# Kernel optimization log

Hardware: AMD Instinct MI355X
Metric: run time of the kernel (lower is better)

Reference implementation:

```python
import jax, jax.numpy as jnp
import numpy as np

THRES1 = 0.8      # self.thres1
THRES_UP = 0.5    # self.thres_up
R = 1.0           # self.r
MAX_FRAME = 60    # self.max_frame
SEQ, FEAT = 65536, 512


def _get_thres2(max_frame=MAX_FRAME, thres=0.6):
    # Faithful port of TGNN.get_threshold: grid-search alpha in (0,1] step 0.01
    a = 0.0
    e = 0.01
    min_score = 1e7
    alpha = e
    for _ in range(100):
        a = a + e
        y = 0.0
        for _ in range(max_frame):
            y = a * 1.0 + (1.0 - a) * y
        score = abs(y - thres)
        if min_score > score:
            min_score = score
            alpha = a
    # with up=1, a_ stays == alpha, so y[i] = alpha + (1-alpha)*y[i-1]
    y = 0.0
    ys = []
    for _ in range(max_frame):
        y = alpha + (1.0 - alpha) * y
        ys.append(y)
    return np.asarray(ys, dtype=np.float32)


def setup_inputs() -> dict:
    key = jax.random.key(0)
    k0, k1, k2, k3, k4 = jax.random.split(key, 5)
    h = jax.random.normal(k0, (SEQ, FEAT), jnp.float32)            # per-frame CTR features
    W = jax.random.normal(k1, (FEAT, 1), jnp.float32) / np.float32(np.sqrt(FEAT))
    b = jnp.zeros((1,), jnp.float32)
    u = jax.random.uniform(k2, (SEQ,), jnp.float32)                # batch['u'] (unused in loss, as in torch)
    u_pred = jax.random.uniform(k3, (SEQ,), jnp.float32)           # batch['u_pred']
    label = jax.random.uniform(k4, (SEQ,), jnp.float32)            # batch['y']
    thres2 = jnp.asarray(_get_thres2())
    return {"h": h, "W": W, "b": b, "u": u, "u_pred": u_pred, "label": label, "thres2": thres2}


def reference(h, W, b, u, u_pred, label, thres2):
    # stand-in for self.ctr.calc_alpha(h).squeeze(): per-frame alpha in (0,1)
    a = jax.nn.sigmoid(h @ W + b)[:, 0]                             # [seq]
    seq = a.shape[0]
    idxs = jnp.arange(seq, dtype=jnp.int32)

    def step(carry, xs):
        up_pre, up_max, a_pre, y_pre, l_c, loss, cnt = carry
        i, a_i, up_i, lab_i = xs
        # start_frame is reset to 0 at the top of every torch iteration, so
        # i - start_frame == 0 whenever start_frame > 0 -> that elif never fires,
        # and in the l_e branch start_frame == 0 -> index is simply i.
        cross = (up_pre < THRES_UP) & (up_i >= THRES_UP)
        up_max = jnp.where(cross, up_i, jnp.maximum(up_max, up_i))
        up_hat = jnp.where(up_i >= THRES_UP, up_max, up_i)
        alpha_ = up_hat * a_pre + (1.0 - up_hat) * a_i
        y_ = alpha_ * up_hat + (1.0 - alpha_) * y_pre
        y_ = jnp.where(up_hat < THRES_UP, jnp.float32(0.0), y_)
        # label >= thres1: set pending loss l_c (sentinel -1 if gate closed)
        l_c = jnp.where(lab_i >= THRES1,
                        jnp.where(up_hat < THRES_UP, jnp.float32(-1.0), (y_ - lab_i) ** 2),
                        l_c)
        # falling edge of the gate: flush accumulated loss
        fall = (up_pre >= THRES_UP) & (up_hat < THRES_UP)
        is_neg = l_c == -1.0
        nonzero = l_c != 0.0
        t2 = thres2[jnp.minimum(i, MAX_FRAME - 1)]
        l_e = (y_pre - t2) ** 2
        add_c = fall & (~is_neg) & nonzero
        add_e = fall & (~is_neg) & (~nonzero) & (y_pre >= THRES1)
        loss = loss + jnp.where(add_c, l_c * R, 0.0) + jnp.where(add_e, l_e, 0.0)
        cnt = cnt + (add_c | add_e).astype(jnp.int32)
        l_c = jnp.where(fall, jnp.float32(0.0), l_c)
        return (up_hat, up_max, alpha_, y_, l_c, loss, cnt), (alpha_, up_hat, y_)

    z = jnp.float32(0.0)
    init = (z, z, z, z, z, z, jnp.int32(0))
    (_, _, _, _, _, loss, cnt), (alphas, up_hats, ys) = jax.lax.scan(
        step, init, (idxs, a, u_pred, label))
    return ys, alphas, u_pred, up_hats, loss, cnt
```

## Files before the change

### kernel.cpp

```cpp
#include <hip/hip_runtime.h>
#include <math.h>

#define SEQ 65536
#define FEAT 512
#define NCH 256
#define CHUNK 256
#define THRES1 0.8f
#define THRES_UP 0.5f
#define NEGINF -1e30f

__global__ __launch_bounds__(256) void k_matvec(const float* __restrict__ h,
                                                const float* __restrict__ W,
                                                const float* __restrict__ b,
                                                float* __restrict__ a) {
    int wave = threadIdx.x >> 6;
    int lane = threadIdx.x & 63;
    int row  = blockIdx.x * 4 + wave;
    const float4* hp = (const float4*)(h + (size_t)row * FEAT);
    const float4* wp = (const float4*)W;
    int base = lane * 2;
    float4 h0 = hp[base], h1 = hp[base + 1];
    float4 w0 = wp[base], w1 = wp[base + 1];
    float s = h0.x * w0.x + h0.y * w0.y + h0.z * w0.z + h0.w * w0.w
            + h1.x * w1.x + h1.y * w1.y + h1.z * w1.z + h1.w * w1.w;
    #pragma unroll
    for (int off = 32; off; off >>= 1) s += __shfl_down(s, off, 64);
    if (lane == 0) a[row] = 1.0f / (1.0f + expf(-(s + b[0])));
}

__global__ __launch_bounds__(256) void k_local(const float* __restrict__ u_pred,
                                               const float* __restrict__ label,
                                               float* __restrict__ m_loc, int* __restrict__ openA,
                                               int* __restrict__ ltLoc, int* __restrict__ lfExcl,
                                               float* __restrict__ lastm, int* __restrict__ lastopen,
                                               int* __restrict__ lastgate, int* __restrict__ trigLast,
                                               int* __restrict__ fallLast) {
    __shared__ float su[256];
    __shared__ float sm[256];
    __shared__ int   sr[256];
    __shared__ int   st[256];
    __shared__ int   sf[256];
    int t = threadIdx.x, c = blockIdx.x;
    int i = c * CHUNK + t;
    float u = u_pred[i];
    su[t] = u;
    __syncthreads();
    bool gate = u >= THRES_UP;
    bool gprevLocal = (t > 0) && (su[t - 1] >= THRES_UP);
    bool gprev = (t > 0) ? gprevLocal : ((i > 0) && (u_pred[i - 1] >= THRES_UP));
    bool fall = gprev && !gate;
    bool trig = label[i] >= THRES1;

    sm[t] = gate ? u : NEGINF;
    sr[t] = gate ? ((t > 0 && !gprevLocal) ? 1 : 0) : 1;
    st[t] = trig ? i : -1;
    sf[t] = fall ? i : -1;
    __syncthreads();
    for (int d = 1; d < 256; d <<= 1) {
        float lm = NEGINF; int lr = 0, lt = -1, lf = -1;
        bool act = t >= d;
        if (act) { lm = sm[t - d]; lr = sr[t - d]; lt = st[t - d]; lf = sf[t - d]; }
        __syncthreads();
        if (act) {
            if (!sr[t]) sm[t] = fmaxf(lm, sm[t]);
            sr[t] |= lr;
            st[t] = max(st[t], lt);
            sf[t] = max(sf[t], lf);
        }
        __syncthreads();
    }
    m_loc[i]  = sm[t];
    openA[i]  = (sr[t] == 0 && gate) ? 1 : 0;
    ltLoc[i]  = st[t];
    lfExcl[i] = (t == 0) ? -1 : sf[t - 1];
    if (t == 255) {
        lastm[c]    = sm[255];
        lastopen[c] = (sr[255] == 0 && gate) ? 1 : 0;
        lastgate[c] = gate ? 1 : 0;
        trigLast[c] = st[255];
        fallLast[c] = sf[255];
    }
}

__global__ __launch_bounds__(256) void k_mid1(const float* __restrict__ lastm,
                                              const int* __restrict__ lastopen,
                                              const int* __restrict__ lastgate,
                                              const int* __restrict__ trigLast,
                                              const int* __restrict__ fallLast,
                                              float* __restrict__ inc, int* __restrict__ trigIn,
                                              int* __restrict__ fallIn,
                                              float* __restrict__ losscnt) {
    __shared__ float sA[256], sB[256];
    __shared__ int   st[256], sf[256];
    int t = threadIdx.x;
    bool lg = lastgate[t] != 0;
    sA[t] = lg ? lastm[t] : NEGINF;
    sB[t] = (lg && lastopen[t]) ? 0.0f : NEGINF;
    st[t] = trigLast[t];
    sf[t] = fallLast[t];
    __syncthreads();
    for (int d = 1; d < 256; d <<= 1) {
        float lA = NEGINF, lB = NEGINF; int lt = -1, lf = -1;
        bool act = t >= d;
        if (act) { lA = sA[t - d]; lB = sB[t - d]; lt = st[t - d]; lf = sf[t - d]; }
        __syncthreads();
        if (act) {
            float nA = fmaxf(sA[t], sB[t] + lA);
            float nB = fmaxf(sB[t] + lB, NEGINF);
            sA[t] = nA; sB[t] = nB;
            st[t] = max(st[t], lt);
            sf[t] = max(sf[t], lf);
        }
        __syncthreads();
    }
    inc[t]    = (t == 0) ? NEGINF : fmaxf(sA[t - 1], sB[t - 1] + NEGINF);
    trigIn[t] = (t == 0) ? -1 : st[t - 1];
    fallIn[t] = (t == 0) ? -1 : sf[t - 1];
    if (t == 0) { losscnt[0] = 0.0f; losscnt[1] = 0.0f; }
}

__global__ __launch_bounds__(256) void k_uphat_alpha(const float* __restrict__ u_pred,
                                                     const float* __restrict__ a,
                                                     const float* __restrict__ m_loc,
                                                     const int* __restrict__ openA,
                                                     const float* __restrict__ inc,
                                                     float* __restrict__ Pc, float* __restrict__ Qc,
                                                     float* __restrict__ Pch, float* __restrict__ Qch,
                                                     float* __restrict__ out) {
    __shared__ float sc[256], sd[256];
    int t = threadIdx.x, c = blockIdx.x;
    int i = c * CHUNK + t;
    float u = u_pred[i];
    bool gate = u >= THRES_UP;
    float uh = gate ? (openA[i] ? fmaxf(m_loc[i], inc[c]) : m_loc[i]) : u;
    out[3 * SEQ + i] = uh;
    out[2 * SEQ + i] = u;
    sc[t] = uh;
    sd[t] = (1.0f - uh) * a[i];
    __syncthreads();
    for (int d = 1; d < 256; d <<= 1) {
        float lc = 1.0f, ld = 0.0f;
        bool act = t >= d;
        if (act) { lc = sc[t - d]; ld = sd[t - d]; }
        __syncthreads();
        if (act) { sd[t] = sc[t] * ld + sd[t]; sc[t] = sc[t] * lc; }
        __syncthreads();
    }
    Pc[i] = sc[t];
    Qc[i] = sd[t];
    if (t == 255) { Pch[c] = sc[255]; Qch[c] = sd[255]; }
}

__global__ __launch_bounds__(256) void k_mid_affine(const float* __restrict__ P,
                                                    const float* __restrict__ Q,
                                                    float* __restrict__ res) {
    __shared__ float sc[256], sd[256];
    int t = threadIdx.x;
    sc[t] = P[t]; sd[t] = Q[t];
    __syncthreads();
    for (int d = 1; d < 256; d <<= 1) {
        float lc = 1.0f, ld = 0.0f;
        bool act = t >= d;
        if (act) { lc = sc[t - d]; ld = sd[t - d]; }
        __syncthreads();
        if (act) { sd[t] = sc[t] * ld + sd[t]; sc[t] = sc[t] * lc; }
        __syncthreads();
    }
    res[t] = (t == 0) ? 0.0f : sd[t - 1];
}

__global__ __launch_bounds__(256) void k_alpha_y(float* __restrict__ Pc, float* __restrict__ Qc,
                                                 const float* __restrict__ alphaIn,
                                                 float* __restrict__ out,
                                                 float* __restrict__ Ech, float* __restrict__ Fch) {
    __shared__ float sc[256], sd[256];
    int t = threadIdx.x, c = blockIdx.x;
    int i = c * CHUNK + t;
    float al = Pc[i] * alphaIn[c] + Qc[i];
    out[SEQ + i] = al;
    float uh = out[3 * SEQ + i];
    bool gate = uh >= THRES_UP;
    sc[t] = gate ? (1.0f - al) : 0.0f;
    sd[t] = gate ? al * uh : 0.0f;
    __syncthreads();
    for (int d = 1; d < 256; d <<= 1) {
        float lc = 1.0f, ld = 0.0f;
        bool act = t >= d;
        if (act) { lc = sc[t - d]; ld = sd[t - d]; }
        __syncthreads();
        if (act) { sd[t] = sc[t] * ld + sd[t]; sc[t] = sc[t] * lc; }
        __syncthreads();
    }
    Pc[i] = sc[t];
    Qc[i] = sd[t];
    if (t == 255) { Ech[c] = sc[255]; Fch[c] = sd[255]; }
}

__global__ __launch_bounds__(256) void k_yfinal(const float* __restrict__ Ec,
                                                const float* __restrict__ Fc,
                                                const float* __restrict__ yIn,
                                                float* __restrict__ out) {
    int t = threadIdx.x, c = blockIdx.x;
    int i = c * CHUNK + t;
    out[i] = Ec[i] * yIn[c] + Fc[i];
}

__global__ __launch_bounds__(256) void k_loss(const float* __restrict__ u_pred,
                                              const float* __restrict__ label,
                                              const float* __restrict__ thres2,
                                              const int* __restrict__ ltLoc,
                                              const int* __restrict__ lfExcl,
                                              const int* __restrict__ trigIn,
                                              const int* __restrict__ fallIn,
                                              const float* __restrict__ y,
                                              float* __restrict__ out) {
    int t = threadIdx.x, c = blockIdx.x;
    int i = c * CHUNK + t;
    float u = u_pred[i];
    bool gate = u >= THRES_UP;
    bool gprev = (i > 0) && (u_pred[i - 1] >= THRES_UP);
    bool fall = gprev && !gate;
    float contrib = 0.0f;
    int flag = 0;
    if (fall) {
        int j  = max(ltLoc[i], trigIn[c]);
        int pf = max(lfExcl[i], fallIn[c]);
        float lc = 0.0f;
        if (j > pf) {
            bool gj = u_pred[j] >= THRES_UP;
            float d = y[j] - label[j];
            lc = gj ? d * d : -1.0f;
        }
        bool isneg = (lc == -1.0f);
        bool nonzero = (lc != 0.0f);
        if (!isneg) {
            if (nonzero) { contrib = lc; flag = 1; }
            else {
                float ypre = y[i - 1];
                if (ypre >= THRES1) {
                    float t2 = thres2[(i < 59) ? i : 59];
                    float d2 = ypre - t2;
                    contrib = d2 * d2; flag = 1;
                }
            }
        }
    }
    #pragma unroll
    for (int off = 32; off; off >>= 1) {
        contrib += __shfl_down(contrib, off, 64);
        flag    += __shfl_down(flag, off, 64);
    }
    if ((t & 63) == 0) {
        atomicAdd(&out[4 * SEQ], contrib);
        atomicAdd(&out[4 * SEQ + 1], (float)flag);
    }
}

extern "C" void kernel_launch(void* const* d_in, const int* in_sizes, int n_in,
                              void* d_out, int out_size, void* d_ws, size_t ws_size,
                              hipStream_t stream) {
    const float* h      = (const float*)d_in[0];
    const float* W      = (const float*)d_in[1];
    const float* b      = (const float*)d_in[2];
    const float* u_pred = (const float*)d_in[4];
    const float* label  = (const float*)d_in[5];
    const float* thres2 = (const float*)d_in[6];
    float* out  = (float*)d_out;
    float* base = (float*)d_ws;

    float* a      = base;
    float* m_loc  = base + SEQ;
    float* Pc     = base + 2 * SEQ;
    float* Qc     = base + 3 * SEQ;
    int*   openA  = (int*)(base + 4 * (size_t)SEQ);
    int*   ltLoc  = (int*)(base + 5 * (size_t)SEQ);
    int*   lfExcl = (int*)(base + 6 * (size_t)SEQ);
    float* sums   = base + 7 * (size_t)SEQ;
    float* lastm   = sums;
    float* Pch     = sums + NCH;
    float* Qch     = sums + 2 * NCH;
    float* inc     = sums + 3 * NCH;
    float* alphaIn = sums + 4 * NCH;
    float* yIn     = sums + 5 * NCH;
    int*   lastopen = (int*)(sums + 6 * NCH);
    int*   lastgate = (int*)(sums + 7 * NCH);
    int*   trigLast = (int*)(sums + 8 * NCH);
    int*   fallLast = (int*)(sums + 9 * NCH);
    int*   trigIn   = (int*)(sums + 10 * NCH);
    int*   fallIn   = (int*)(sums + 11 * NCH);

    k_matvec<<<SEQ / 4, 256, 0, stream>>>(h, W, b, a);
    k_local<<<NCH, CHUNK, 0, stream>>>(u_pred, label, m_loc, openA, ltLoc, lfExcl,
                                       lastm, lastopen, lastgate, trigLast, fallLast);
    k_mid1<<<1, NCH, 0, stream>>>(lastm, lastopen, lastgate, trigLast, fallLast,
                                  inc, trigIn, fallIn, out + 4 * SEQ);
    k_uphat_alpha<<<NCH, CHUNK, 0, stream>>>(u_pred, a, m_loc, openA, inc, Pc, Qc, Pch, Qch, out);
    k_mid_affine<<<1, NCH, 0, stream>>>(Pch, Qch, alphaIn);
    k_alpha_y<<<NCH, CHUNK, 0, stream>>>(Pc, Qc, alphaIn, out, Pch, Qch);
    k_mid_affine<<<1, NCH, 0, stream>>>(Pch, Qch, yIn);
    k_yfinal<<<NCH, CHUNK, 0, stream>>>(Pc, Qc, yIn, out);
    k_loss<<<NCH, CHUNK, 0, stream>>>(u_pred, label, thres2, ltLoc, lfExcl, trigIn, fallIn, out, out);
}
```

Before: 246.4 us.

## Fuse scan pipeline into a single cooperative kernel with grid syncs

Replaces the eight post-matvec launches (local scans, single-block mid scans, y computation, loss) with one cooperative kernel that keeps per-element intermediates in registers. Every block redundantly scans the 256 chunk carries after each grid.sync. This removes launch gaps, serial single-block kernels and global round trips of intermediate arrays. In exchange it depends on cooperative launch with all 256 blocks co-resident, adds four grid-wide barriers, and skips the loss atomics for waves whose sums are zero.

New measurement: 431.6 us. 1.75x slower.

```diff
diff --git a/kernel.cpp b/kernel.cpp
--- a/kernel.cpp
+++ b/kernel.cpp
@@ -1,5 +1,8 @@
 #include <hip/hip_runtime.h>
+#include <hip/hip_cooperative_groups.h>
 #include <math.h>
+
+namespace cg = cooperative_groups;
 
 #define SEQ 65536
 #define FEAT 512
@@ -28,207 +31,158 @@
     if (lane == 0) a[row] = 1.0f / (1.0f + expf(-(s + b[0])));
 }
 
-__global__ __launch_bounds__(256) void k_local(const float* __restrict__ u_pred,
-                                               const float* __restrict__ label,
-                                               float* __restrict__ m_loc, int* __restrict__ openA,
-                                               int* __restrict__ ltLoc, int* __restrict__ lfExcl,
-                                               float* __restrict__ lastm, int* __restrict__ lastopen,
-                                               int* __restrict__ lastgate, int* __restrict__ trigLast,
-                                               int* __restrict__ fallLast) {
-    __shared__ float su[256];
-    __shared__ float sm[256];
-    __shared__ int   sr[256];
-    __shared__ int   st[256];
-    __shared__ int   sf[256];
+__device__ __forceinline__ void affine_scan256(float* sc, float* sd, int t) {
+    for (int d = 1; d < 256; d <<= 1) {
+        float lc = 1.0f, ld = 0.0f;
+        bool act = t >= d;
+        if (act) { lc = sc[t - d]; ld = sd[t - d]; }
+        __syncthreads();
+        if (act) { sd[t] = sc[t] * ld + sd[t]; sc[t] = sc[t] * lc; }
+        __syncthreads();
+    }
+}
+
+__global__ __launch_bounds__(256) void k_scan(const float* __restrict__ u_pred,
+                                              const float* __restrict__ label,
+                                              const float* __restrict__ thres2,
+                                              const float* __restrict__ a,
+                                              float* __restrict__ out,
+                                              float* __restrict__ sf_,
+                                              int* __restrict__ si_) {
+    cg::grid_group grid = cg::this_grid();
+    __shared__ float sA[256], sB[256], sU[256];
+    __shared__ int   iA[256], iB[256], iC[256];
+
     int t = threadIdx.x, c = blockIdx.x;
     int i = c * CHUNK + t;
-    float u = u_pred[i];
-    su[t] = u;
+
+    float* lastm = sf_;
+    float* Pch   = sf_ + NCH;
+    float* Qch   = sf_ + 2 * NCH;
+    float* Ech   = sf_ + 3 * NCH;
+    float* Fch   = sf_ + 4 * NCH;
+    int* lastopen = si_;
+    int* lastgate = si_ + NCH;
+    int* trigLast = si_ + 2 * NCH;
+    int* fallLast = si_ + 3 * NCH;
+
+    float u   = u_pred[i];
+    float lab = label[i];
+    float a_i = a[i];
+    sU[t] = u;
     __syncthreads();
     bool gate = u >= THRES_UP;
-    bool gprevLocal = (t > 0) && (su[t - 1] >= THRES_UP);
+    bool gprevLocal = (t > 0) && (sU[t - 1] >= THRES_UP);
     bool gprev = (t > 0) ? gprevLocal : ((i > 0) && (u_pred[i - 1] >= THRES_UP));
     bool fall = gprev && !gate;
-    bool trig = label[i] >= THRES1;
-
-    sm[t] = gate ? u : NEGINF;
-    sr[t] = gate ? ((t > 0 && !gprevLocal) ? 1 : 0) : 1;
-    st[t] = trig ? i : -1;
-    sf[t] = fall ? i : -1;
+    bool trig = lab >= THRES1;
+
+    sA[t] = gate ? u : NEGINF;
+    iA[t] = gate ? ((t > 0 && !gprevLocal) ? 1 : 0) : 1;
+    iB[t] = trig ? i : -1;
+    iC[t] = fall ? i : -1;
     __syncthreads();
     for (int d = 1; d < 256; d <<= 1) {
-        float lm = NEGINF; int lr = 0, lt = -1, lf = -1;
+        float lm = NEGINF; int lr = 0, lt_ = -1, lf_ = -1;
         bool act = t >= d;
-        if (act) { lm = sm[t - d]; lr = sr[t - d]; lt = st[t - d]; lf = sf[t - d]; }
+        if (act) { lm = sA[t - d]; lr = iA[t - d]; lt_ = iB[t - d]; lf_ = iC[t - d]; }
         __syncthreads();
         if (act) {
-            if (!sr[t]) sm[t] = fmaxf(lm, sm[t]);
-            sr[t] |= lr;
-            st[t] = max(st[t], lt);
-            sf[t] = max(sf[t], lf);
-        }
-        __syncthreads();
-    }
-    m_loc[i]  = sm[t];
-    openA[i]  = (sr[t] == 0 && gate) ? 1 : 0;
-    ltLoc[i]  = st[t];
-    lfExcl[i] = (t == 0) ? -1 : sf[t - 1];
+            if (!iA[t]) sA[t] = fmaxf(lm, sA[t]);
+            iA[t] |= lr;
+            iB[t] = max(iB[t], lt_);
+            iC[t] = max(iC[t], lf_);
+        }
+        __syncthreads();
+    }
+    float m_loc = sA[t];
+    int   open  = (iA[t] == 0 && gate) ? 1 : 0;
+    int   lt    = iB[t];
+    int   lfE   = (t == 0) ? -1 : iC[t - 1];
     if (t == 255) {
-        lastm[c]    = sm[255];
-        lastopen[c] = (sr[255] == 0 && gate) ? 1 : 0;
+        lastm[c]    = sA[255];
+        lastopen[c] = open;
         lastgate[c] = gate ? 1 : 0;
-        trigLast[c] = st[255];
-        fallLast[c] = sf[255];
-    }
-}
-
-__global__ __launch_bounds__(256) void k_mid1(const float* __restrict__ lastm,
-                                              const int* __restrict__ lastopen,
-                                              const int* __restrict__ lastgate,
-                                              const int* __restrict__ trigLast,
-                                              const int* __restrict__ fallLast,
-                                              float* __restrict__ inc, int* __restrict__ trigIn,
-                                              int* __restrict__ fallIn,
-                                              float* __restrict__ losscnt) {
-    __shared__ float sA[256], sB[256];
-    __shared__ int   st[256], sf[256];
-    int t = threadIdx.x;
-    bool lg = lastgate[t] != 0;
-    sA[t] = lg ? lastm[t] : NEGINF;
-    sB[t] = (lg && lastopen[t]) ? 0.0f : NEGINF;
-    st[t] = trigLast[t];
-    sf[t] = fallLast[t];
+        trigLast[c] = iB[255];
+        fallLast[c] = iC[255];
+    }
+    if (c == 0 && t == 0) { out[4 * SEQ] = 0.0f; out[4 * SEQ + 1] = 0.0f; }
+    __threadfence();
+    grid.sync();
+
+    {
+        bool lg = lastgate[t] != 0;
+        sA[t] = lg ? lastm[t] : NEGINF;
+        sB[t] = (lg && lastopen[t]) ? 0.0f : NEGINF;
+        iA[t] = trigLast[t];
+        iB[t] = fallLast[t];
+    }
     __syncthreads();
     for (int d = 1; d < 256; d <<= 1) {
-        float lA = NEGINF, lB = NEGINF; int lt = -1, lf = -1;
+        float lA = NEGINF, lB = NEGINF; int lt_ = -1, lf_ = -1;
         bool act = t >= d;
-        if (act) { lA = sA[t - d]; lB = sB[t - d]; lt = st[t - d]; lf = sf[t - d]; }
+        if (act) { lA = sA[t - d]; lB = sB[t - d]; lt_ = iA[t - d]; lf_ = iB[t - d]; }
         __syncthreads();
         if (act) {
             float nA = fmaxf(sA[t], sB[t] + lA);
             float nB = fmaxf(sB[t] + lB, NEGINF);
             sA[t] = nA; sB[t] = nB;
-            st[t] = max(st[t], lt);
-            sf[t] = max(sf[t], lf);
-        }
-        __syncthreads();
-    }
-    inc[t]    = (t == 0) ? NEGINF : fmaxf(sA[t - 1], sB[t - 1] + NEGINF);
-    trigIn[t] = (t == 0) ? -1 : st[t - 1];
-    fallIn[t] = (t == 0) ? -1 : sf[t - 1];
-    if (t == 0) { losscnt[0] = 0.0f; losscnt[1] = 0.0f; }
-}
-
-__global__ __launch_bounds__(256) void k_uphat_alpha(const float* __restrict__ u_pred,
-                                                     const float* __restrict__ a,
-                                                     const float* __restrict__ m_loc,
-                                                     const int* __restrict__ openA,
-                                                     const float* __restrict__ inc,
-                                                     float* __restrict__ Pc, float* __restrict__ Qc,
-                                                     float* __restrict__ Pch, float* __restrict__ Qch,
-                                                     float* __restrict__ out) {
-    __shared__ float sc[256], sd[256];
-    int t = threadIdx.x, c = blockIdx.x;
-    int i = c * CHUNK + t;
-    float u = u_pred[i];
-    bool gate = u >= THRES_UP;
-    float uh = gate ? (openA[i] ? fmaxf(m_loc[i], inc[c]) : m_loc[i]) : u;
+            iA[t] = max(iA[t], lt_);
+            iB[t] = max(iB[t], lf_);
+        }
+        __syncthreads();
+    }
+    float inc_c; int trigIn_c, fallIn_c;
+    if (c == 0) { inc_c = NEGINF; trigIn_c = -1; fallIn_c = -1; }
+    else        { inc_c = sA[c - 1]; trigIn_c = iA[c - 1]; fallIn_c = iB[c - 1]; }
+    __syncthreads();
+
+    float uh = gate ? (open ? fmaxf(m_loc, inc_c) : m_loc) : u;
     out[3 * SEQ + i] = uh;
     out[2 * SEQ + i] = u;
-    sc[t] = uh;
-    sd[t] = (1.0f - uh) * a[i];
-    __syncthreads();
-    for (int d = 1; d < 256; d <<= 1) {
-        float lc = 1.0f, ld = 0.0f;
-        bool act = t >= d;
-        if (act) { lc = sc[t - d]; ld = sd[t - d]; }
-        __syncthreads();
-        if (act) { sd[t] = sc[t] * ld + sd[t]; sc[t] = sc[t] * lc; }
-        __syncthreads();
-    }
-    Pc[i] = sc[t];
-    Qc[i] = sd[t];
-    if (t == 255) { Pch[c] = sc[255]; Qch[c] = sd[255]; }
-}
-
-__global__ __launch_bounds__(256) void k_mid_affine(const float* __restrict__ P,
-                                                    const float* __restrict__ Q,
-                                                    float* __restrict__ res) {
-    __shared__ float sc[256], sd[256];
-    int t = threadIdx.x;
-    sc[t] = P[t]; sd[t] = Q[t];
-    __syncthreads();
-    for (int d = 1; d < 256; d <<= 1) {
-        float lc = 1.0f, ld = 0.0f;
-        bool act = t >= d;
-        if (act) { lc = sc[t - d]; ld = sd[t - d]; }
-        __syncthreads();
-        if (act) { sd[t] = sc[t] * ld + sd[t]; sc[t] = sc[t] * lc; }
-        __syncthreads();
-    }
-    res[t] = (t == 0) ? 0.0f : sd[t - 1];
-}
-
-__global__ __launch_bounds__(256) void k_alpha_y(float* __restrict__ Pc, float* __restrict__ Qc,
-                                                 const float* __restrict__ alphaIn,
-                                                 float* __restrict__ out,
-                                                 float* __restrict__ Ech, float* __restrict__ Fch) {
-    __shared__ float sc[256], sd[256];
-    int t = threadIdx.x, c = blockIdx.x;
-    int i = c * CHUNK + t;
-    float al = Pc[i] * alphaIn[c] + Qc[i];
+    sA[t] = uh;
+    sB[t] = (1.0f - uh) * a_i;
+    __syncthreads();
+    affine_scan256(sA, sB, t);
+    float Pt = sA[t], Qt = sB[t];
+    if (t == 255) { Pch[c] = Pt; Qch[c] = Qt; }
+    __threadfence();
+    grid.sync();
+
+    sA[t] = Pch[t]; sB[t] = Qch[t];
+    __syncthreads();
+    affine_scan256(sA, sB, t);
+    float alphaIn_c = (c == 0) ? 0.0f : sB[c - 1];
+    __syncthreads();
+    float al = Pt * alphaIn_c + Qt;
     out[SEQ + i] = al;
-    float uh = out[3 * SEQ + i];
-    bool gate = uh >= THRES_UP;
-    sc[t] = gate ? (1.0f - al) : 0.0f;
-    sd[t] = gate ? al * uh : 0.0f;
-    __syncthreads();
-    for (int d = 1; d < 256; d <<= 1) {
-        float lc = 1.0f, ld = 0.0f;
-        bool act = t >= d;
-        if (act) { lc = sc[t - d]; ld = sd[t - d]; }
-        __syncthreads();
-        if (act) { sd[t] = sc[t] * ld + sd[t]; sc[t] = sc[t] * lc; }
-        __syncthreads();
-    }
-    Pc[i] = sc[t];
-    Qc[i] = sd[t];
-    if (t == 255) { Ech[c] = sc[255]; Fch[c] = sd[255]; }
-}
-
-__global__ __launch_bounds__(256) void k_yfinal(const float* __restrict__ Ec,
-                                                const float* __restrict__ Fc,
-                                                const float* __restrict__ yIn,
-                                                float* __restrict__ out) {
-    int t = threadIdx.x, c = blockIdx.x;
-    int i = c * CHUNK + t;
-    out[i] = Ec[i] * yIn[c] + Fc[i];
-}
-
-__global__ __launch_bounds__(256) void k_loss(const float* __restrict__ u_pred,
-                                              const float* __restrict__ label,
-                                              const float* __restrict__ thres2,
-                                              const int* __restrict__ ltLoc,
-                                              const int* __restrict__ lfExcl,
-                                              const int* __restrict__ trigIn,
-                                              const int* __restrict__ fallIn,
-                                              const float* __restrict__ y,
-                                              float* __restrict__ out) {
-    int t = threadIdx.x, c = blockIdx.x;
-    int i = c * CHUNK + t;
-    float u = u_pred[i];
-    bool gate = u >= THRES_UP;
-    bool gprev = (i > 0) && (u_pred[i - 1] >= THRES_UP);
-    bool fall = gprev && !gate;
+    sA[t] = gate ? (1.0f - al) : 0.0f;
+    sB[t] = gate ? al * uh : 0.0f;
+    __syncthreads();
+    affine_scan256(sA, sB, t);
+    float Et = sA[t], Ft = sB[t];
+    if (t == 255) { Ech[c] = Et; Fch[c] = Ft; }
+    __threadfence();
+    grid.sync();
+
+    sA[t] = Ech[t]; sB[t] = Fch[t];
+    __syncthreads();
+    affine_scan256(sA, sB, t);
+    float yIn_c = (c == 0) ? 0.0f : sB[c - 1];
+    float y_i = Et * yIn_c + Ft;
+    out[i] = y_i;
+    __threadfence();
+    grid.sync();
+
     float contrib = 0.0f;
     int flag = 0;
     if (fall) {
-        int j  = max(ltLoc[i], trigIn[c]);
-        int pf = max(lfExcl[i], fallIn[c]);
+        int j  = max(lt, trigIn_c);
+        int pf = max(lfE, fallIn_c);
         float lc = 0.0f;
         if (j > pf) {
             bool gj = u_pred[j] >= THRES_UP;
-            float d = y[j] - label[j];
+            float d = out[j] - label[j];
             lc = gj ? d * d : -1.0f;
         }
         bool isneg = (lc == -1.0f);
@@ -236,7 +190,7 @@
         if (!isneg) {
             if (nonzero) { contrib = lc; flag = 1; }
             else {
-                float ypre = y[i - 1];
+                float ypre = out[i - 1];
                 if (ypre >= THRES1) {
                     float t2 = thres2[(i < 59) ? i : 59];
                     float d2 = ypre - t2;
@@ -250,7 +204,7 @@
         contrib += __shfl_down(contrib, off, 64);
         flag    += __shfl_down(flag, off, 64);
     }
-    if ((t & 63) == 0) {
+    if ((t & 63) == 0 && (contrib != 0.0f || flag != 0)) {
         atomicAdd(&out[4 * SEQ], contrib);
         atomicAdd(&out[4 * SEQ + 1], (float)flag);
     }
@@ -268,36 +222,13 @@
     float* out  = (float*)d_out;
     float* base = (float*)d_ws;
 
-    float* a      = base;
-    float* m_loc  = base + SEQ;
-    float* Pc     = base + 2 * SEQ;
-    float* Qc     = base + 3 * SEQ;
-    int*   openA  = (int*)(base + 4 * (size_t)SEQ);
-    int*   ltLoc  = (int*)(base + 5 * (size_t)SEQ);
-    int*   lfExcl = (int*)(base + 6 * (size_t)SEQ);
-    float* sums   = base + 7 * (size_t)SEQ;
-    float* lastm   = sums;
-    float* Pch     = sums + NCH;
-    float* Qch     = sums + 2 * NCH;
-    float* inc     = sums + 3 * NCH;
-    float* alphaIn = sums + 4 * NCH;
-    float* yIn     = sums + 5 * NCH;
-    int*   lastopen = (int*)(sums + 6 * NCH);
-    int*   lastgate = (int*)(sums + 7 * NCH);
-    int*   trigLast = (int*)(sums + 8 * NCH);
-    int*   fallLast = (int*)(sums + 9 * NCH);
-    int*   trigIn   = (int*)(sums + 10 * NCH);
-    int*   fallIn   = (int*)(sums + 11 * NCH);
+    float* a   = base;
+    float* sf_ = base + SEQ;
+    int*   si_ = (int*)(base + SEQ + 5 * NCH);
 
     k_matvec<<<SEQ / 4, 256, 0, stream>>>(h, W, b, a);
-    k_local<<<NCH, CHUNK, 0, stream>>>(u_pred, label, m_loc, openA, ltLoc, lfExcl,
-                                       lastm, lastopen, lastgate, trigLast, fallLast);
-    k_mid1<<<1, NCH, 0, stream>>>(lastm, lastopen, lastgate, trigLast, fallLast,
-                                  inc, trigIn, fallIn, out + 4 * SEQ);
-    k_uphat_alpha<<<NCH, CHUNK, 0, stream>>>(u_pred, a, m_loc, openA, inc, Pc, Qc, Pch, Qch, out);
-    k_mid_affine<<<1, NCH, 0, stream>>>(Pch, Qch, alphaIn);
-    k_alpha_y<<<NCH, CHUNK, 0, stream>>>(Pc, Qc, alphaIn, out, Pch, Qch);
-    k_mid_affine<<<1, NCH, 0, stream>>>(Pch, Qch, yIn);
-    k_yfinal<<<NCH, CHUNK, 0, stream>>>(Pc, Qc, yIn, out);
-    k_loss<<<NCH, CHUNK, 0, stream>>>(u_pred, label, thres2, ltLoc, lfExcl, trigIn, fallIn, out, out);
-}
+
+    void* args[] = { (void*)&u_pred, (void*)&label, (void*)&thres2, (void*)&a,
+                     (void*)&out, (void*)&sf_, (void*)&si_ };
+    hipLaunchCooperativeKernel((void*)k_scan, dim3(NCH), dim3(256), args, 0, stream);
+}
```
